# Kernel tuning notes

Measured on AMD Instinct MI355X. Metric: run time of the kernel, lower is better.

## Reference

```python
import jax, jax.numpy as jnp
import numpy as np

N_NODES = 100000
N_EDGES = 1600000
D_FEAT = 64


def setup_inputs() -> dict:
    key = jax.random.key(0)
    k1, k2, k3 = jax.random.split(key, 3)
    adj_indices = jax.random.randint(k1, (2, N_EDGES), 0, N_NODES, dtype=jnp.int64 if jax.config.jax_enable_x64 else jnp.int32)
    # symmetric-normalized-like edge weights in (0, 1)
    adj_values = jax.random.uniform(k2, (N_EDGES,), dtype=jnp.float32)
    feats = jax.random.normal(k3, (N_NODES, D_FEAT), dtype=jnp.float32)
    return {"adj_indices": adj_indices, "adj_values": adj_values, "feats": feats}


def reference(adj_indices, adj_values, feats):
    """out = sparse_adj @ feats  (COO SpMM via gather + segment_sum).

    adj_indices: [2, E] int (row, col) coordinates of nonzeros
    adj_values : [E] float nonzero values
    feats      : [N, d] dense node features
    returns    : [N, d]
    """
    rows = adj_indices[0]
    cols = adj_indices[1]
    # gather neighbor features, scale by edge weight: [E, d]
    msgs = adj_values[:, None] * feats[cols]
    # scatter-add into destination rows: [N, d]
    return jax.ops.segment_sum(msgs, rows, num_segments=feats.shape[0])
```

## Files before the change

### kernel.cpp

```cpp
#include <hip/hip_runtime.h>

#define NN 100000
#define NE 1600000
#define DF 64
#define RPB 32
#define NBS 3328
#define NBU 3125
#define OFS_STRIDE (NBS + 1)
#define CHK 4096
#define SCAP 768
#define SPB 13

__device__ inline float bflo(unsigned int u) { return __uint_as_float(u << 16); }
__device__ inline float bfhi(unsigned int u) { return __uint_as_float(u & 0xFFFF0000u); }

__device__ inline unsigned int bfpack(float lo, float hi) {
    unsigned int ul = __float_as_uint(lo), uh = __float_as_uint(hi);
    ul = (ul + 0x7FFFu + ((ul >> 16) & 1u)) >> 16;
    uh = (uh + 0x7FFFu + ((uh >> 16) & 1u)) & 0xFFFF0000u;
    return ul | uh;
}

__global__ __launch_bounds__(256) void cvt_kernel(const float* __restrict__ feats,
                                                  uint4* __restrict__ fbf) {
    int t = blockIdx.x * blockDim.x + threadIdx.x;
    if (t >= NN * DF / 8) return;
    const float4* f4 = reinterpret_cast<const float4*>(feats);
    float4 a = f4[2 * t];
    float4 b = f4[2 * t + 1];
    uint4 o;
    o.x = bfpack(a.x, a.y);
    o.y = bfpack(a.z, a.w);
    o.z = bfpack(b.x, b.y);
    o.w = bfpack(b.z, b.w);
    fbf[t] = o;
}

__global__ __launch_bounds__(256) void part_kernel(
    const int* __restrict__ rows, const int* __restrict__ cols,
    const float* __restrict__ vals, unsigned short* __restrict__ ofs,
    int2* __restrict__ packed, int E)
{
    int c = blockIdx.x;
    int base = c * CHK;
    int n = E - base; if (n > CHK) n = CHK;
    int t = threadIdx.x;

    __shared__ int cnt[NBS];
    __shared__ int cnt2[NBS];
    __shared__ int scanv[NBS];
    __shared__ int tsum[256];

    for (int b = t; b < NBS; b += 256) { cnt[b] = 0; cnt2[b] = 0; }
    __syncthreads();

    int rr[16]; int cc[16]; float vv[16];
#pragma unroll
    for (int k = 0; k < 16; ++k) {
        int i = t + k * 256;
        if (i < n) {
            rr[k] = rows[base + i];
            cc[k] = cols[base + i];
            vv[k] = vals[base + i];
            atomicAdd(&cnt[rr[k] >> 5], 1);
        }
    }
    __syncthreads();

    int local[SPB]; int s = 0;
#pragma unroll
    for (int j = 0; j < SPB; ++j) { local[j] = cnt[t * SPB + j]; s += local[j]; }
    tsum[t] = s;
    __syncthreads();
    for (int d = 1; d < 256; d <<= 1) {
        int x = (t >= d) ? tsum[t - d] : 0;
        __syncthreads();
        tsum[t] += x;
        __syncthreads();
    }
    int run = tsum[t] - s;
#pragma unroll
    for (int j = 0; j < SPB; ++j) { scanv[t * SPB + j] = run; run += local[j]; }
    __syncthreads();

    unsigned short* og = ofs + (size_t)c * OFS_STRIDE;
    for (int b = t; b < NBS; b += 256) og[b] = (unsigned short)scanv[b];
    if (t == 0) og[NBS] = (unsigned short)n;

#pragma unroll
    for (int k = 0; k < 16; ++k) {
        int i = t + k * 256;
        if (i < n) {
            int r = rr[k];
            int b = r >> 5;
            int rank = atomicAdd(&cnt2[b], 1);
            int pos = base + scanv[b] + rank;
            packed[pos] = make_int2(cc[k] | ((r & 31) << 17), __float_as_int(vv[k]));
        }
    }
}

__global__ __launch_bounds__(256) void spmm_kernel(
    const unsigned short* __restrict__ ofs, const int2* __restrict__ packed,
    const unsigned short* __restrict__ fbf, float* __restrict__ out, int nc)
{
    int borig = blockIdx.x;
    int xcd = borig & 7;
    int sub = borig >> 3;
    int b = (xcd < 5 ? xcd * 391 : 5 * 391 + (xcd - 5) * 390) + sub;

    int t = threadIdx.x;

    __shared__ int2 sorted[SCAP];
    __shared__ int cnt[RPB];
    __shared__ int rstart[RPB + 1];

    if (t < RPB) cnt[t] = 0;
    __syncthreads();

    int c2 = t + 256;
    int sA = 0, eA = 0, sB = 0, eB = 0;
    if (t < nc) {
        const unsigned short* og = ofs + (size_t)t * OFS_STRIDE + b;
        sA = og[0]; eA = og[1];
    }
    if (c2 < nc) {
        const unsigned short* og = ofs + (size_t)c2 * OFS_STRIDE + b;
        sB = og[0]; eB = og[1];
    }
    int lenA = eA - sA, lenB = eB - sB;

    int2 ebA[8], ebB[8];
#pragma unroll
    for (int k = 0; k < 8; ++k) if (k < lenA) ebA[k] = packed[t * CHK + sA + k];
#pragma unroll
    for (int k = 0; k < 8; ++k) if (k < lenB) ebB[k] = packed[c2 * CHK + sB + k];

#pragma unroll
    for (int k = 0; k < 8; ++k) if (k < lenA) atomicAdd(&cnt[(ebA[k].x >> 17) & 31], 1);
    for (int i = sA + 8; i < eA; ++i) atomicAdd(&cnt[(packed[t * CHK + i].x >> 17) & 31], 1);
#pragma unroll
    for (int k = 0; k < 8; ++k) if (k < lenB) atomicAdd(&cnt[(ebB[k].x >> 17) & 31], 1);
    for (int i = sB + 8; i < eB; ++i) atomicAdd(&cnt[(packed[c2 * CHK + i].x >> 17) & 31], 1);
    __syncthreads();

    if (t < RPB) {
        int v = cnt[t];
        int incl = v;
        for (int d = 1; d < RPB; d <<= 1) {
            int x = __shfl_up(incl, d, 64);
            if (t >= d) incl += x;
        }
        rstart[t] = incl - v;
        if (t == RPB - 1) rstart[RPB] = incl;
    }
    __syncthreads();
    if (t < RPB) cnt[t] = rstart[t];
    __syncthreads();

#pragma unroll
    for (int k = 0; k < 8; ++k) if (k < lenA) {
        int rl = (ebA[k].x >> 17) & 31;
        int pos = atomicAdd(&cnt[rl], 1);
        if (pos < SCAP) sorted[pos] = make_int2(ebA[k].x & 0x1FFFF, ebA[k].y);
    }
    for (int i = sA + 8; i < eA; ++i) {
        int2 cv = packed[t * CHK + i];
        int rl = (cv.x >> 17) & 31;
        int pos = atomicAdd(&cnt[rl], 1);
        if (pos < SCAP) sorted[pos] = make_int2(cv.x & 0x1FFFF, cv.y);
    }
#pragma unroll
    for (int k = 0; k < 8; ++k) if (k < lenB) {
        int rl = (ebB[k].x >> 17) & 31;
        int pos = atomicAdd(&cnt[rl], 1);
        if (pos < SCAP) sorted[pos] = make_int2(ebB[k].x & 0x1FFFF, ebB[k].y);
    }
    for (int i = sB + 8; i < eB; ++i) {
        int2 cv = packed[c2 * CHK + i];
        int rl = (cv.x >> 17) & 31;
        int pos = atomicAdd(&cnt[rl], 1);
        if (pos < SCAP) sorted[pos] = make_int2(cv.x & 0x1FFFF, cv.y);
    }
    __syncthreads();

    int w = t >> 6;
    int lane = t & 63;
    int grp = lane >> 4;
    int fq = lane & 15;
    int rowbase = b * RPB;

    for (int rl = w * 8; rl < w * 8 + 8; ++rl) {
        int row = rowbase + rl;
        int beg = rstart[rl], end = rstart[rl + 1];
        float4 acc = make_float4(0.f, 0.f, 0.f, 0.f);
        int i = beg + grp;
        for (; i + 12 < end; i += 16) {
            int2 e0 = sorted[i];
            int2 e1 = sorted[i + 4];
            int2 e2 = sorted[i + 8];
            int2 e3 = sorted[i + 12];
            const uint2 g0 = *reinterpret_cast<const uint2*>(fbf + (size_t)e0.x * DF + fq * 4);
            const uint2 g1 = *reinterpret_cast<const uint2*>(fbf + (size_t)e1.x * DF + fq * 4);
            const uint2 g2 = *reinterpret_cast<const uint2*>(fbf + (size_t)e2.x * DF + fq * 4);
            const uint2 g3 = *reinterpret_cast<const uint2*>(fbf + (size_t)e3.x * DF + fq * 4);
            float v0 = __int_as_float(e0.y), v1 = __int_as_float(e1.y);
            float v2 = __int_as_float(e2.y), v3 = __int_as_float(e3.y);
            acc.x += v0 * bflo(g0.x); acc.y += v0 * bfhi(g0.x);
            acc.z += v0 * bflo(g0.y); acc.w += v0 * bfhi(g0.y);
            acc.x += v1 * bflo(g1.x); acc.y += v1 * bfhi(g1.x);
            acc.z += v1 * bflo(g1.y); acc.w += v1 * bfhi(g1.y);
            acc.x += v2 * bflo(g2.x); acc.y += v2 * bfhi(g2.x);
            acc.z += v2 * bflo(g2.y); acc.w += v2 * bfhi(g2.y);
            acc.x += v3 * bflo(g3.x); acc.y += v3 * bfhi(g3.x);
            acc.z += v3 * bflo(g3.y); acc.w += v3 * bfhi(g3.y);
        }
        for (; i + 4 < end; i += 8) {
            int2 e0 = sorted[i];
            int2 e1 = sorted[i + 4];
            const uint2 g0 = *reinterpret_cast<const uint2*>(fbf + (size_t)e0.x * DF + fq * 4);
            const uint2 g1 = *reinterpret_cast<const uint2*>(fbf + (size_t)e1.x * DF + fq * 4);
            float v0 = __int_as_float(e0.y), v1 = __int_as_float(e1.y);
            acc.x += v0 * bflo(g0.x); acc.y += v0 * bfhi(g0.x);
            acc.z += v0 * bflo(g0.y); acc.w += v0 * bfhi(g0.y);
            acc.x += v1 * bflo(g1.x); acc.y += v1 * bfhi(g1.x);
            acc.z += v1 * bflo(g1.y); acc.w += v1 * bfhi(g1.y);
        }
        if (i < end) {
            int2 e0 = sorted[i];
            const uint2 g0 = *reinterpret_cast<const uint2*>(fbf + (size_t)e0.x * DF + fq * 4);
            float v0 = __int_as_float(e0.y);
            acc.x += v0 * bflo(g0.x); acc.y += v0 * bfhi(g0.x);
            acc.z += v0 * bflo(g0.y); acc.w += v0 * bfhi(g0.y);
        }
#pragma unroll
        for (int m = 16; m <= 32; m <<= 1) {
            acc.x += __shfl_xor(acc.x, m, 64);
            acc.y += __shfl_xor(acc.y, m, 64);
            acc.z += __shfl_xor(acc.z, m, 64);
            acc.w += __shfl_xor(acc.w, m, 64);
        }
        if (grp == 0 && row < NN)
            *reinterpret_cast<float4*>(out + (size_t)row * DF + fq * 4) = acc;
    }
}


extern "C" void kernel_launch(void* const* d_in, const int* in_sizes, int n_in,
                              void* d_out, int out_size, void* d_ws, size_t ws_size,
                              hipStream_t stream) {
    const int* adj_indices = (const int*)d_in[0];
    const float* adj_values = (const float*)d_in[1];
    const float* feats = (const float*)d_in[2];
    float* out = (float*)d_out;

    const int E = in_sizes[1];
    const int* rows = adj_indices;
    const int* cols = adj_indices + E;

    const int nc = (E + CHK - 1) / CHK;

    unsigned short* fbf = (unsigned short*)d_ws;
    size_t fbf_bytes = (size_t)NN * DF * 2;
    unsigned short* ofs = (unsigned short*)((char*)d_ws + fbf_bytes);
    size_t ofs_bytes = (size_t)nc * OFS_STRIDE * 2;
    size_t packed_off = (fbf_bytes + ofs_bytes + 15) & ~(size_t)15;
    int2* packed = (int2*)((char*)d_ws + packed_off);

    cvt_kernel<<<(NN * DF / 8 + 255) / 256, 256, 0, stream>>>(feats, (uint4*)fbf);
    part_kernel<<<nc, 256, 0, stream>>>(rows, cols, adj_values, ofs, packed, E);
    spmm_kernel<<<NBU, 256, 0, stream>>>(ofs, packed, fbf, out, nc);
}
```

Before: 69.70 us.

## Fuse bf16 conversion into partition kernel, halve chunk size, pair-row gather loop

Merges the feature bf16 conversion and the edge partition into one launch, with extra blocks doing the conversion in a grid-stride loop. Halves the partition chunk size so twice as many chunks spread the work over more blocks and use less register and shared state. The old second counter array is replaced by atomics on the scan array. The spmm kernel now reads four chunk segments per thread, and its gather loop handles two rows at once with predicated loads to expose more memory-level parallelism. The cost is more per-block segment reads and wasted predicated lanes for short rows.

New measurement: 69.37 us. About the same (-0.5%).

```diff
diff --git a/kernel.cpp b/kernel.cpp
--- a/kernel.cpp
+++ b/kernel.cpp
@@ -7,7 +7,10 @@
 #define NBS 3328
 #define NBU 3125
 #define OFS_STRIDE (NBS + 1)
-#define CHK 4096
+#define CHK 2048
+#define NC 782
+#define CVTB 1024
+#define CVT_N (NN * DF / 8)
 #define SCAP 768
 #define SPB 13
 
@@ -21,42 +24,43 @@
     return ul | uh;
 }
 
-__global__ __launch_bounds__(256) void cvt_kernel(const float* __restrict__ feats,
-                                                  uint4* __restrict__ fbf) {
-    int t = blockIdx.x * blockDim.x + threadIdx.x;
-    if (t >= NN * DF / 8) return;
-    const float4* f4 = reinterpret_cast<const float4*>(feats);
-    float4 a = f4[2 * t];
-    float4 b = f4[2 * t + 1];
-    uint4 o;
-    o.x = bfpack(a.x, a.y);
-    o.y = bfpack(a.z, a.w);
-    o.z = bfpack(b.x, b.y);
-    o.w = bfpack(b.z, b.w);
-    fbf[t] = o;
-}
-
-__global__ __launch_bounds__(256) void part_kernel(
+__global__ __launch_bounds__(256) void prep_kernel(
     const int* __restrict__ rows, const int* __restrict__ cols,
-    const float* __restrict__ vals, unsigned short* __restrict__ ofs,
-    int2* __restrict__ packed, int E)
+    const float* __restrict__ vals, const float* __restrict__ feats,
+    unsigned short* __restrict__ ofs, int2* __restrict__ packed,
+    uint4* __restrict__ fbf, int E)
 {
+    __shared__ int cnt[NBS];
+    __shared__ int scanv[NBS];
+    __shared__ int tsum[256];
+
+    int t = threadIdx.x;
+
+    if (blockIdx.x >= NC) {
+        const float4* f4 = reinterpret_cast<const float4*>(feats);
+        for (int idx = (blockIdx.x - NC) * 256 + t; idx < CVT_N; idx += CVTB * 256) {
+            float4 a = f4[2 * idx];
+            float4 b = f4[2 * idx + 1];
+            uint4 o;
+            o.x = bfpack(a.x, a.y);
+            o.y = bfpack(a.z, a.w);
+            o.z = bfpack(b.x, b.y);
+            o.w = bfpack(b.z, b.w);
+            fbf[idx] = o;
+        }
+        return;
+    }
+
     int c = blockIdx.x;
     int base = c * CHK;
     int n = E - base; if (n > CHK) n = CHK;
-    int t = threadIdx.x;
-
-    __shared__ int cnt[NBS];
-    __shared__ int cnt2[NBS];
-    __shared__ int scanv[NBS];
-    __shared__ int tsum[256];
-
-    for (int b = t; b < NBS; b += 256) { cnt[b] = 0; cnt2[b] = 0; }
-    __syncthreads();
-
-    int rr[16]; int cc[16]; float vv[16];
-#pragma unroll
-    for (int k = 0; k < 16; ++k) {
+
+    for (int b = t; b < NBS; b += 256) cnt[b] = 0;
+    __syncthreads();
+
+    int rr[8]; int cc[8]; float vv[8];
+#pragma unroll
+    for (int k = 0; k < 8; ++k) {
         int i = t + k * 256;
         if (i < n) {
             rr[k] = rows[base + i];
@@ -86,15 +90,14 @@
     unsigned short* og = ofs + (size_t)c * OFS_STRIDE;
     for (int b = t; b < NBS; b += 256) og[b] = (unsigned short)scanv[b];
     if (t == 0) og[NBS] = (unsigned short)n;
-
-#pragma unroll
-    for (int k = 0; k < 16; ++k) {
+    __syncthreads();
+
+#pragma unroll
+    for (int k = 0; k < 8; ++k) {
         int i = t + k * 256;
         if (i < n) {
             int r = rr[k];
-            int b = r >> 5;
-            int rank = atomicAdd(&cnt2[b], 1);
-            int pos = base + scanv[b] + rank;
+            int pos = base + atomicAdd(&scanv[r >> 5], 1);
             packed[pos] = make_int2(cc[k] | ((r & 31) << 17), __float_as_int(vv[k]));
         }
     }
@@ -118,30 +121,31 @@
     if (t < RPB) cnt[t] = 0;
     __syncthreads();
 
-    int c2 = t + 256;
-    int sA = 0, eA = 0, sB = 0, eB = 0;
-    if (t < nc) {
-        const unsigned short* og = ofs + (size_t)t * OFS_STRIDE + b;
-        sA = og[0]; eA = og[1];
-    }
-    if (c2 < nc) {
-        const unsigned short* og = ofs + (size_t)c2 * OFS_STRIDE + b;
-        sB = og[0]; eB = og[1];
-    }
-    int lenA = eA - sA, lenB = eB - sB;
-
-    int2 ebA[8], ebB[8];
-#pragma unroll
-    for (int k = 0; k < 8; ++k) if (k < lenA) ebA[k] = packed[t * CHK + sA + k];
-#pragma unroll
-    for (int k = 0; k < 8; ++k) if (k < lenB) ebB[k] = packed[c2 * CHK + sB + k];
-
-#pragma unroll
-    for (int k = 0; k < 8; ++k) if (k < lenA) atomicAdd(&cnt[(ebA[k].x >> 17) & 31], 1);
-    for (int i = sA + 8; i < eA; ++i) atomicAdd(&cnt[(packed[t * CHK + i].x >> 17) & 31], 1);
-#pragma unroll
-    for (int k = 0; k < 8; ++k) if (k < lenB) atomicAdd(&cnt[(ebB[k].x >> 17) & 31], 1);
-    for (int i = sB + 8; i < eB; ++i) atomicAdd(&cnt[(packed[c2 * CHK + i].x >> 17) & 31], 1);
+    int segS[4], segE[4];
+    int2 eb[16];
+#pragma unroll
+    for (int q = 0; q < 4; ++q) {
+        int cseg = t + q * 256;
+        int s = 0, e = 0;
+        if (cseg < nc) {
+            const unsigned short* og = ofs + (size_t)cseg * OFS_STRIDE + b;
+            s = og[0]; e = og[1];
+        }
+        segS[q] = s; segE[q] = e;
+#pragma unroll
+        for (int k = 0; k < 4; ++k)
+            if (s + k < e) eb[q * 4 + k] = packed[cseg * CHK + s + k];
+    }
+
+#pragma unroll
+    for (int q = 0; q < 4; ++q) {
+#pragma unroll
+        for (int k = 0; k < 4; ++k)
+            if (segS[q] + k < segE[q])
+                atomicAdd(&cnt[(eb[q * 4 + k].x >> 17) & 31], 1);
+        for (int i = segS[q] + 4; i < segE[q]; ++i)
+            atomicAdd(&cnt[(packed[(t + q * 256) * CHK + i].x >> 17) & 31], 1);
+    }
     __syncthreads();
 
     if (t < RPB) {
@@ -159,28 +163,21 @@
     __syncthreads();
 
 #pragma unroll
-    for (int k = 0; k < 8; ++k) if (k < lenA) {
-        int rl = (ebA[k].x >> 17) & 31;
-        int pos = atomicAdd(&cnt[rl], 1);
-        if (pos < SCAP) sorted[pos] = make_int2(ebA[k].x & 0x1FFFF, ebA[k].y);
-    }
-    for (int i = sA + 8; i < eA; ++i) {
-        int2 cv = packed[t * CHK + i];
-        int rl = (cv.x >> 17) & 31;
-        int pos = atomicAdd(&cnt[rl], 1);
-        if (pos < SCAP) sorted[pos] = make_int2(cv.x & 0x1FFFF, cv.y);
-    }
-#pragma unroll
-    for (int k = 0; k < 8; ++k) if (k < lenB) {
-        int rl = (ebB[k].x >> 17) & 31;
-        int pos = atomicAdd(&cnt[rl], 1);
-        if (pos < SCAP) sorted[pos] = make_int2(ebB[k].x & 0x1FFFF, ebB[k].y);
-    }
-    for (int i = sB + 8; i < eB; ++i) {
-        int2 cv = packed[c2 * CHK + i];
-        int rl = (cv.x >> 17) & 31;
-        int pos = atomicAdd(&cnt[rl], 1);
-        if (pos < SCAP) sorted[pos] = make_int2(cv.x & 0x1FFFF, cv.y);
+    for (int q = 0; q < 4; ++q) {
+#pragma unroll
+        for (int k = 0; k < 4; ++k)
+            if (segS[q] + k < segE[q]) {
+                int2 cv = eb[q * 4 + k];
+                int rl = (cv.x >> 17) & 31;
+                int pos = atomicAdd(&cnt[rl], 1);
+                if (pos < SCAP) sorted[pos] = make_int2(cv.x & 0x1FFFF, cv.y);
+            }
+        for (int i = segS[q] + 4; i < segE[q]; ++i) {
+            int2 cv = packed[(t + q * 256) * CHK + i];
+            int rl = (cv.x >> 17) & 31;
+            int pos = atomicAdd(&cnt[rl], 1);
+            if (pos < SCAP) sorted[pos] = make_int2(cv.x & 0x1FFFF, cv.y);
+        }
     }
     __syncthreads();
 
@@ -190,58 +187,76 @@
     int fq = lane & 15;
     int rowbase = b * RPB;
 
-    for (int rl = w * 8; rl < w * 8 + 8; ++rl) {
-        int row = rowbase + rl;
-        int beg = rstart[rl], end = rstart[rl + 1];
-        float4 acc = make_float4(0.f, 0.f, 0.f, 0.f);
-        int i = beg + grp;
-        for (; i + 12 < end; i += 16) {
-            int2 e0 = sorted[i];
-            int2 e1 = sorted[i + 4];
-            int2 e2 = sorted[i + 8];
-            int2 e3 = sorted[i + 12];
-            const uint2 g0 = *reinterpret_cast<const uint2*>(fbf + (size_t)e0.x * DF + fq * 4);
-            const uint2 g1 = *reinterpret_cast<const uint2*>(fbf + (size_t)e1.x * DF + fq * 4);
-            const uint2 g2 = *reinterpret_cast<const uint2*>(fbf + (size_t)e2.x * DF + fq * 4);
-            const uint2 g3 = *reinterpret_cast<const uint2*>(fbf + (size_t)e3.x * DF + fq * 4);
-            float v0 = __int_as_float(e0.y), v1 = __int_as_float(e1.y);
-            float v2 = __int_as_float(e2.y), v3 = __int_as_float(e3.y);
-            acc.x += v0 * bflo(g0.x); acc.y += v0 * bfhi(g0.x);
-            acc.z += v0 * bflo(g0.y); acc.w += v0 * bfhi(g0.y);
-            acc.x += v1 * bflo(g1.x); acc.y += v1 * bfhi(g1.x);
-            acc.z += v1 * bflo(g1.y); acc.w += v1 * bfhi(g1.y);
-            acc.x += v2 * bflo(g2.x); acc.y += v2 * bfhi(g2.x);
-            acc.z += v2 * bflo(g2.y); acc.w += v2 * bfhi(g2.y);
-            acc.x += v3 * bflo(g3.x); acc.y += v3 * bfhi(g3.x);
-            acc.z += v3 * bflo(g3.y); acc.w += v3 * bfhi(g3.y);
-        }
-        for (; i + 4 < end; i += 8) {
-            int2 e0 = sorted[i];
-            int2 e1 = sorted[i + 4];
-            const uint2 g0 = *reinterpret_cast<const uint2*>(fbf + (size_t)e0.x * DF + fq * 4);
-            const uint2 g1 = *reinterpret_cast<const uint2*>(fbf + (size_t)e1.x * DF + fq * 4);
-            float v0 = __int_as_float(e0.y), v1 = __int_as_float(e1.y);
-            acc.x += v0 * bflo(g0.x); acc.y += v0 * bfhi(g0.x);
-            acc.z += v0 * bflo(g0.y); acc.w += v0 * bfhi(g0.y);
-            acc.x += v1 * bflo(g1.x); acc.y += v1 * bfhi(g1.x);
-            acc.z += v1 * bflo(g1.y); acc.w += v1 * bfhi(g1.y);
-        }
-        if (i < end) {
-            int2 e0 = sorted[i];
-            const uint2 g0 = *reinterpret_cast<const uint2*>(fbf + (size_t)e0.x * DF + fq * 4);
-            float v0 = __int_as_float(e0.y);
-            acc.x += v0 * bflo(g0.x); acc.y += v0 * bfhi(g0.x);
-            acc.z += v0 * bflo(g0.y); acc.w += v0 * bfhi(g0.y);
+#pragma unroll
+    for (int rp = 0; rp < 4; ++rp) {
+        int rl = w * 8 + rp * 2;
+        int beg0 = rstart[rl],     end0 = rstart[rl + 1];
+        int beg1 = rstart[rl + 1], end1 = rstart[rl + 2];
+        float4 acc0 = make_float4(0.f, 0.f, 0.f, 0.f);
+        float4 acc1 = make_float4(0.f, 0.f, 0.f, 0.f);
+        int i0 = beg0 + grp, i1 = beg1 + grp;
+        while (i0 < end0 || i1 < end1) {
+            bool v00 = i0      < end0, v01 = i0 + 4  < end0;
+            bool v02 = i0 + 8  < end0, v03 = i0 + 12 < end0;
+            bool v10 = i1      < end1, v11 = i1 + 4  < end1;
+            bool v12 = i1 + 8  < end1, v13 = i1 + 12 < end1;
+            int2 E00 = sorted[v00 ? i0      : 0];
+            int2 E01 = sorted[v01 ? i0 + 4  : 0];
+            int2 E02 = sorted[v02 ? i0 + 8  : 0];
+            int2 E03 = sorted[v03 ? i0 + 12 : 0];
+            int2 E10 = sorted[v10 ? i1      : 0];
+            int2 E11 = sorted[v11 ? i1 + 4  : 0];
+            int2 E12 = sorted[v12 ? i1 + 8  : 0];
+            int2 E13 = sorted[v13 ? i1 + 12 : 0];
+            const uint2 G00 = *reinterpret_cast<const uint2*>(fbf + (size_t)(E00.x & 0x1FFFF) * DF + fq * 4);
+            const uint2 G01 = *reinterpret_cast<const uint2*>(fbf + (size_t)(E01.x & 0x1FFFF) * DF + fq * 4);
+            const uint2 G02 = *reinterpret_cast<const uint2*>(fbf + (size_t)(E02.x & 0x1FFFF) * DF + fq * 4);
+            const uint2 G03 = *reinterpret_cast<const uint2*>(fbf + (size_t)(E03.x & 0x1FFFF) * DF + fq * 4);
+            const uint2 G10 = *reinterpret_cast<const uint2*>(fbf + (size_t)(E10.x & 0x1FFFF) * DF + fq * 4);
+            const uint2 G11 = *reinterpret_cast<const uint2*>(fbf + (size_t)(E11.x & 0x1FFFF) * DF + fq * 4);
+            const uint2 G12 = *reinterpret_cast<const uint2*>(fbf + (size_t)(E12.x & 0x1FFFF) * DF + fq * 4);
+            const uint2 G13 = *reinterpret_cast<const uint2*>(fbf + (size_t)(E13.x & 0x1FFFF) * DF + fq * 4);
+            if (v00) { float v = __int_as_float(E00.y);
+                acc0.x += v * bflo(G00.x); acc0.y += v * bfhi(G00.x);
+                acc0.z += v * bflo(G00.y); acc0.w += v * bfhi(G00.y); }
+            if (v01) { float v = __int_as_float(E01.y);
+                acc0.x += v * bflo(G01.x); acc0.y += v * bfhi(G01.x);
+                acc0.z += v * bflo(G01.y); acc0.w += v * bfhi(G01.y); }
+            if (v02) { float v = __int_as_float(E02.y);
+                acc0.x += v * bflo(G02.x); acc0.y += v * bfhi(G02.x);
+                acc0.z += v * bflo(G02.y); acc0.w += v * bfhi(G02.y); }
+            if (v03) { float v = __int_as_float(E03.y);
+                acc0.x += v * bflo(G03.x); acc0.y += v * bfhi(G03.x);
+                acc0.z += v * bflo(G03.y); acc0.w += v * bfhi(G03.y); }
+            if (v10) { float v = __int_as_float(E10.y);
+                acc1.x += v * bflo(G10.x); acc1.y += v * bfhi(G10.x);
+                acc1.z += v * bflo(G10.y); acc1.w += v * bfhi(G10.y); }
+            if (v11) { float v = __int_as_float(E11.y);
+                acc1.x += v * bflo(G11.x); acc1.y += v * bfhi(G11.x);
+                acc1.z += v * bflo(G11.y); acc1.w += v * bfhi(G11.y); }
+            if (v12) { float v = __int_as_float(E12.y);
+                acc1.x += v * bflo(G12.x); acc1.y += v * bfhi(G12.x);
+                acc1.z += v * bflo(G12.y); acc1.w += v * bfhi(G12.y); }
+            if (v13) { float v = __int_as_float(E13.y);
+                acc1.x += v * bflo(G13.x); acc1.y += v * bfhi(G13.x);
+                acc1.z += v * bflo(G13.y); acc1.w += v * bfhi(G13.y); }
+            i0 += 16; i1 += 16;
         }
 #pragma unroll
         for (int m = 16; m <= 32; m <<= 1) {
-            acc.x += __shfl_xor(acc.x, m, 64);
-            acc.y += __shfl_xor(acc.y, m, 64);
-            acc.z += __shfl_xor(acc.z, m, 64);
-            acc.w += __shfl_xor(acc.w, m, 64);
-        }
-        if (grp == 0 && row < NN)
-            *reinterpret_cast<float4*>(out + (size_t)row * DF + fq * 4) = acc;
+            acc0.x += __shfl_xor(acc0.x, m, 64);
+            acc0.y += __shfl_xor(acc0.y, m, 64);
+            acc0.z += __shfl_xor(acc0.z, m, 64);
+            acc0.w += __shfl_xor(acc0.w, m, 64);
+            acc1.x += __shfl_xor(acc1.x, m, 64);
+            acc1.y += __shfl_xor(acc1.y, m, 64);
+            acc1.z += __shfl_xor(acc1.z, m, 64);
+            acc1.w += __shfl_xor(acc1.w, m, 64);
+        }
+        if (grp == 0) {
+            *reinterpret_cast<float4*>(out + (size_t)(rowbase + rl) * DF + fq * 4) = acc0;
+            *reinterpret_cast<float4*>(out + (size_t)(rowbase + rl + 1) * DF + fq * 4) = acc1;
+        }
     }
 }
 
@@ -258,16 +273,14 @@
     const int* rows = adj_indices;
     const int* cols = adj_indices + E;
 
-    const int nc = (E + CHK - 1) / CHK;
-
     unsigned short* fbf = (unsigned short*)d_ws;
     size_t fbf_bytes = (size_t)NN * DF * 2;
     unsigned short* ofs = (unsigned short*)((char*)d_ws + fbf_bytes);
-    size_t ofs_bytes = (size_t)nc * OFS_STRIDE * 2;
+    size_t ofs_bytes = (size_t)NC * OFS_STRIDE * 2;
     size_t packed_off = (fbf_bytes + ofs_bytes + 15) & ~(size_t)15;
     int2* packed = (int2*)((char*)d_ws + packed_off);
 
-    cvt_kernel<<<(NN * DF / 8 + 255) / 256, 256, 0, stream>>>(feats, (uint4*)fbf);
-    part_kernel<<<nc, 256, 0, stream>>>(rows, cols, adj_values, ofs, packed, E);
-    spmm_kernel<<<NBU, 256, 0, stream>>>(ofs, packed, fbf, out, nc);
-}
+    prep_kernel<<<NC + CVTB, 256, 0, stream>>>(rows, cols, adj_values, feats,
+                                               ofs, packed, (uint4*)fbf, E);
+    spmm_kernel<<<NBU, 256, 0, stream>>>(ofs, packed, fbf, out, NC);
+}
```

## Fuse bf16 conversion into partition kernel and reuse scan array for ranks

Applied to the files above, without the earlier changes.

Merges the feature bf16 conversion kernel and the edge partition kernel into a single launch, where extra blocks beyond the partition chunks do a grid-stride conversion. This removes one kernel launch and lets the two independent prep phases run concurrently. It also drops the second shared counter array by atomically incrementing the scanned offsets directly, which saves shared memory and may raise occupancy. The row bounds check in the SpMM store is removed, and the chunk count is hard-coded to the fixed edge count.

New measurement: 65.24 us. 1.07x faster.

```diff
diff --git a/kernel.cpp b/kernel.cpp
--- a/kernel.cpp
+++ b/kernel.cpp
@@ -8,6 +8,9 @@
 #define NBU 3125
 #define OFS_STRIDE (NBS + 1)
 #define CHK 4096
+#define NC 391
+#define CVTB 1024
+#define CVT_N (NN * DF / 8)
 #define SCAP 768
 #define SPB 13
 
@@ -21,37 +24,38 @@
     return ul | uh;
 }
 
-__global__ __launch_bounds__(256) void cvt_kernel(const float* __restrict__ feats,
-                                                  uint4* __restrict__ fbf) {
-    int t = blockIdx.x * blockDim.x + threadIdx.x;
-    if (t >= NN * DF / 8) return;
-    const float4* f4 = reinterpret_cast<const float4*>(feats);
-    float4 a = f4[2 * t];
-    float4 b = f4[2 * t + 1];
-    uint4 o;
-    o.x = bfpack(a.x, a.y);
-    o.y = bfpack(a.z, a.w);
-    o.z = bfpack(b.x, b.y);
-    o.w = bfpack(b.z, b.w);
-    fbf[t] = o;
-}
-
-__global__ __launch_bounds__(256) void part_kernel(
+__global__ __launch_bounds__(256) void prep_kernel(
     const int* __restrict__ rows, const int* __restrict__ cols,
-    const float* __restrict__ vals, unsigned short* __restrict__ ofs,
-    int2* __restrict__ packed, int E)
+    const float* __restrict__ vals, const float* __restrict__ feats,
+    unsigned short* __restrict__ ofs, int2* __restrict__ packed,
+    uint4* __restrict__ fbf, int E)
 {
+    __shared__ int cnt[NBS];
+    __shared__ int scanv[NBS];
+    __shared__ int tsum[256];
+
+    int t = threadIdx.x;
+
+    if (blockIdx.x >= NC) {
+        const float4* f4 = reinterpret_cast<const float4*>(feats);
+        for (int idx = (blockIdx.x - NC) * 256 + t; idx < CVT_N; idx += CVTB * 256) {
+            float4 a = f4[2 * idx];
+            float4 b = f4[2 * idx + 1];
+            uint4 o;
+            o.x = bfpack(a.x, a.y);
+            o.y = bfpack(a.z, a.w);
+            o.z = bfpack(b.x, b.y);
+            o.w = bfpack(b.z, b.w);
+            fbf[idx] = o;
+        }
+        return;
+    }
+
     int c = blockIdx.x;
     int base = c * CHK;
     int n = E - base; if (n > CHK) n = CHK;
-    int t = threadIdx.x;
-
-    __shared__ int cnt[NBS];
-    __shared__ int cnt2[NBS];
-    __shared__ int scanv[NBS];
-    __shared__ int tsum[256];
-
-    for (int b = t; b < NBS; b += 256) { cnt[b] = 0; cnt2[b] = 0; }
+
+    for (int b = t; b < NBS; b += 256) cnt[b] = 0;
     __syncthreads();
 
     int rr[16]; int cc[16]; float vv[16];
@@ -86,15 +90,14 @@
     unsigned short* og = ofs + (size_t)c * OFS_STRIDE;
     for (int b = t; b < NBS; b += 256) og[b] = (unsigned short)scanv[b];
     if (t == 0) og[NBS] = (unsigned short)n;
+    __syncthreads();
 
 #pragma unroll
     for (int k = 0; k < 16; ++k) {
         int i = t + k * 256;
         if (i < n) {
             int r = rr[k];
-            int b = r >> 5;
-            int rank = atomicAdd(&cnt2[b], 1);
-            int pos = base + scanv[b] + rank;
+            int pos = base + atomicAdd(&scanv[r >> 5], 1);
             packed[pos] = make_int2(cc[k] | ((r & 31) << 17), __float_as_int(vv[k]));
         }
     }
@@ -240,7 +243,7 @@
             acc.z += __shfl_xor(acc.z, m, 64);
             acc.w += __shfl_xor(acc.w, m, 64);
         }
-        if (grp == 0 && row < NN)
+        if (grp == 0)
             *reinterpret_cast<float4*>(out + (size_t)row * DF + fq * 4) = acc;
     }
 }
@@ -258,16 +261,14 @@
     const int* rows = adj_indices;
     const int* cols = adj_indices + E;
 
-    const int nc = (E + CHK - 1) / CHK;
-
     unsigned short* fbf = (unsigned short*)d_ws;
     size_t fbf_bytes = (size_t)NN * DF * 2;
     unsigned short* ofs = (unsigned short*)((char*)d_ws + fbf_bytes);
-    size_t ofs_bytes = (size_t)nc * OFS_STRIDE * 2;
+    size_t ofs_bytes = (size_t)NC * OFS_STRIDE * 2;
     size_t packed_off = (fbf_bytes + ofs_bytes + 15) & ~(size_t)15;
     int2* packed = (int2*)((char*)d_ws + packed_off);
 
-    cvt_kernel<<<(NN * DF / 8 + 255) / 256, 256, 0, stream>>>(feats, (uint4*)fbf);
-    part_kernel<<<nc, 256, 0, stream>>>(rows, cols, adj_values, ofs, packed, E);
-    spmm_kernel<<<NBU, 256, 0, stream>>>(ofs, packed, fbf, out, nc);
-}
+    prep_kernel<<<NC + CVTB, 256, 0, stream>>>(rows, cols, adj_values, feats,
+                                               ofs, packed, (uint4*)fbf, E);
+    spmm_kernel<<<NBU, 256, 0, stream>>>(ofs, packed, fbf, out, NC);
+}
```
